# Kernel tuning notes

Measured on AMD Instinct MI355X. Metric: run time of the kernel, lower is better.

## Reference

```python
import jax, jax.numpy as jnp
import numpy as np

HEAD_CHOICES = [8, 10, 12]
MAX_HEADS = 12
HEAD_DIM = 64
MAX_REL_POS = 14
SCALE = HEAD_DIM ** -0.5


def _rel_indices(N):
    # AutoFormer RelativePosition2D_super index computation (static, numpy).
    L = N - 1                      # remove cls token
    s = int(L ** 0.5)              # patches per row
    r = np.arange(L)
    dv = r[None, :] // s - r[:, None] // s
    dh = r[None, :] % s - r[:, None] % s
    iv = np.clip(dv, -MAX_REL_POS, MAX_REL_POS) + MAX_REL_POS + 1
    ih = np.clip(dh, -MAX_REL_POS, MAX_REL_POS) + MAX_REL_POS + 1
    iv = np.pad(iv, ((1, 0), (1, 0)))  # cls token row/col -> index 0
    ih = np.pad(ih, ((1, 0), (1, 0)))
    return jnp.asarray(iv), jnp.asarray(ih)


def setup_inputs() -> dict:
    key = jax.random.key(0)
    ks = jax.random.split(key, 6)
    B, N = 16, 577
    T = 2 * MAX_REL_POS + 2  # 30
    x = jax.random.normal(ks[0], (B, N, 3 * MAX_HEADS * HEAD_DIM), dtype=jnp.float32)
    weights = jax.nn.softmax(jax.random.normal(ks[1], (len(HEAD_CHOICES),), dtype=jnp.float32))
    rel_k_table_v = jax.random.normal(ks[2], (T, HEAD_DIM), dtype=jnp.float32) * 0.02
    rel_k_table_h = jax.random.normal(ks[3], (T, HEAD_DIM), dtype=jnp.float32) * 0.02
    rel_v_table_v = jax.random.normal(ks[4], (T, HEAD_DIM), dtype=jnp.float32) * 0.02
    rel_v_table_h = jax.random.normal(ks[5], (T, HEAD_DIM), dtype=jnp.float32) * 0.02
    return dict(x=x, weights=weights,
                rel_k_table_v=rel_k_table_v, rel_k_table_h=rel_k_table_h,
                rel_v_table_v=rel_v_table_v, rel_v_table_h=rel_v_table_h)


def reference(x, weights, rel_k_table_v, rel_k_table_h, rel_v_table_v, rel_v_table_h):
    B, N, _ = x.shape
    # [3, B, H, N, D]
    qkv = x.reshape(B, N, 3, MAX_HEADS, HEAD_DIM).transpose(2, 0, 3, 1, 4)
    # Mixture over head-count choices: slicing first c heads, scaling by w[i],
    # padding to max_heads, and summing == per-head weight sum_i w[i]*[h < c_i].
    head_mask = jnp.asarray(np.array([[1.0 if h < c else 0.0 for h in range(MAX_HEADS)]
                                      for c in HEAD_CHOICES]), dtype=x.dtype)  # [C, H]
    w_head = weights @ head_mask  # [H]
    w4 = w_head[None, :, None, None]
    q = qkv[0] * w4
    k = qkv[1] * w4
    v = qkv[2] * w4
    # content attention + relative-position K bias
    attn = jnp.einsum('bhnd,bhmd->bhnm', q, k) * SCALE
    iv, ih = _rel_indices(N)
    rel_k = rel_k_table_v[iv] + rel_k_table_h[ih]  # [N, N, D]
    attn = attn + jnp.einsum('bhnd,nmd->bhnm', q, rel_k) * SCALE
    attn = jax.nn.softmax(attn, axis=-1)  # attn_drop has p=0 (eval)
    out = jnp.einsum('bhnm,bhmd->bhnd', attn, v)
    rel_v = rel_v_table_v[iv] + rel_v_table_h[ih]  # [N, N, D]
    out = out + jnp.einsum('bhnm,nmd->bhnd', attn, rel_v)
    return out.transpose(0, 2, 1, 3).reshape(B, N, MAX_HEADS * HEAD_DIM)
```

## Files before the change

kernel.cpp:

```cpp
#include <hip/hip_runtime.h>

typedef short bf16x8_t __attribute__((ext_vector_type(8)));
typedef float f32x4_t __attribute__((ext_vector_type(4)));

#define NTOK 577
#define QPAD 640
#define MPAD 608
#define NSTEP 19
#define VTILES 80
#define VTILE_ELEMS 6144

__device__ __forceinline__ unsigned short f2bf(float f) {
  unsigned u = __builtin_bit_cast(unsigned, f);
  u += 0x7FFFu + ((u >> 16) & 1u);
  return (unsigned short)(u >> 16);
}
__device__ __forceinline__ float headw(const float* wts, int h) {
  float w0 = wts[0], w1 = wts[1], w2 = wts[2];
  return (h < 8) ? (w0 + w1 + w2) : ((h < 10) ? (w1 + w2) : w2);
}
__device__ __forceinline__ unsigned rangemask(int lo, int hi) {
  lo = lo < 0 ? 0 : lo; hi = hi > 32 ? 32 : hi;
  if (hi <= lo) return 0u;
  unsigned mh = (hi >= 32) ? 0xFFFFFFFFu : ((1u << hi) - 1u);
  unsigned ml = (1u << lo) - 1u;
  return mh & ~ml;
}

extern "C" __global__ __launch_bounds__(256) void prep_x3(
    const float* __restrict__ x, const float* __restrict__ wts,
    unsigned short* __restrict__ qbf, unsigned short* __restrict__ kbf,
    unsigned short* __restrict__ vbf) {
  __shared__ unsigned short vT[8][768];
  const int tid = threadIdx.x;
  const int mc = blockIdx.x;
  const int n0 = mc * 8;
  const int b = blockIdx.y;
  const float w0 = wts[0], w1 = wts[1], w2 = wts[2];
  const float wA = w0 + w1 + w2, wB = w1 + w2, wC = w2;
  const float* xb = x + (size_t)b * NTOK * 2304;
#pragma unroll 2
  for (int p = 0; p < 18; ++p) {
    int i = p * 256 + tid;
    int nl = i / 576;
    int c4 = i - nl * 576;
    int n = n0 + nl;
    float4 v = {0.f, 0.f, 0.f, 0.f};
    if (n < NTOK) v = *(const float4*)(xb + (size_t)n * 2304 + c4 * 4);
    int sec = c4 / 192;
    int cc = c4 - sec * 192;
    int h = cc >> 4, d4 = cc & 15;
    if (sec == 2) {
      ushort4 o;
      o.x = f2bf(v.x); o.y = f2bf(v.y); o.z = f2bf(v.z); o.w = f2bf(v.w);
      *(ushort4*)&vT[nl][cc * 4] = o;
    } else {
      float s = 1.f;
      if (sec == 0) {
        float w = (h < 8) ? wA : ((h < 10) ? wB : wC);
        s = w * w * 0.125f;
      }
      ushort4 o;
      o.x = f2bf(v.x * s); o.y = f2bf(v.y * s); o.z = f2bf(v.z * s); o.w = f2bf(v.w * s);
      unsigned short* dst = (sec == 0) ? qbf : kbf;
      *(ushort4*)(dst + ((size_t)(b * 12 + h)) * QPAD * 64 + (size_t)n * 64 + d4 * 4) = o;
    }
  }
  __syncthreads();
  unsigned short* tile = vbf + (size_t)(b * VTILES + mc) * VTILE_ELEMS;
#pragma unroll
  for (int t = 0; t < 3; ++t) {
    int hd = t * 256 + tid;
    bf16x8_t val;
#pragma unroll
    for (int jj = 0; jj < 8; ++jj) val[jj] = (short)vT[jj][hd];
    *(bf16x8_t*)(tile + (size_t)hd * 8) = val;
  }
}

extern "C" __global__ __launch_bounds__(256) void prep_tab(
    const float* __restrict__ wts,
    const float* __restrict__ tkv, const float* __restrict__ tkh,
    const float* __restrict__ tvv, const float* __restrict__ tvh,
    unsigned short* __restrict__ tkb, unsigned short* __restrict__ tvb,
    unsigned short* __restrict__ gfb) {
  int tid = threadIdx.x, bx = blockIdx.x;
  if (bx < 48) {
    int cid = bx * 256 + tid;
    int d4 = cid & 15, t = (cid >> 4) & 31, tb = (cid >> 9) & 1, h = cid >> 10;
    float s = 1.f / headw(wts, h);
    const float* src = tb ? tkh : tkv;
    float4 v = {0,0,0,0};
    if (t < 30) v = *(const float4*)(src + t * 64 + d4 * 4);
    ushort4 o;
    o.x = f2bf(v.x * s); o.y = f2bf(v.y * s); o.z = f2bf(v.z * s); o.w = f2bf(v.w * s);
    *(ushort4*)(tkb + (((size_t)(h * 2 + tb)) * 32 + t) * 64 + d4 * 4) = o;
  } else if (bx == 48) {
    for (int i = 0; i < 16; ++i) {
      int id = tid * 16 + i;
      int t = id & 31, d = (id >> 5) & 63, tb = id >> 11;
      const float* src = tb ? tvh : tvv;
      tvb[id] = (t < 30) ? f2bf(src[t * 64 + d]) : (unsigned short)0;
    }
  } else {
    int id = (bx - 49) * 256 + tid;
    int lane = id & 63, gt = (id >> 6) & 1;
    int sg = id >> 7;
    int step = sg % 19, tb = sg / 19;
    int l15 = lane & 15, quad = lane >> 4;
    int g = gt * 16 + l15;
    int m0 = step * 32;
    unsigned mask = 0u;
    if (g < 25) {
      if (g == 24) {
        mask = rangemask(NTOK - m0, MPAD - m0);
        if (step == 0) mask |= 1u;
      } else if (tb == 0) {
        mask = rangemask(24 * g + 1 - m0, 24 * g + 25 - m0);
      } else {
        int j0 = (g + 1 - m0) % 24; if (j0 < 0) j0 += 24;
        for (int j = j0; j < 32; j += 24) {
          int m = m0 + j;
          if (m >= 1 && m < NTOK) mask |= (1u << j);
        }
      }
    }
    unsigned short o[8];
#pragma unroll
    for (int j = 0; j < 8; ++j) {
      int m_loc = quad * 8 + j;
      o[j] = ((mask >> m_loc) & 1u) ? (unsigned short)0x3F80 : (unsigned short)0;
    }
    *(ushort4*)(gfb + (size_t)id * 8) = *(ushort4*)&o[0];
    *(ushort4*)(gfb + (size_t)id * 8 + 4) = *(ushort4*)&o[4];
  }
}

struct __align__(16) SMem {
  float qg_t[2][25][68];
  float l_s[64];
  union {
    struct { float qv_t[2][64][30]; } pro;
    struct { unsigned short P_s[2][64][44]; } loop;
    struct { float sv_f[2][64][30]; } epi;
  } u;
};

extern "C" __global__ __launch_bounds__(256, 4) void hma_kernel(
    const unsigned short* __restrict__ qbf, const unsigned short* __restrict__ kbf,
    const unsigned short* __restrict__ vbf, const unsigned short* __restrict__ tkb,
    const unsigned short* __restrict__ tvb, const unsigned short* __restrict__ gfb,
    const float* __restrict__ wts, float* __restrict__ out) {
  __shared__ SMem sm;
  const int tid = threadIdx.x;
  const int wave = tid >> 6, lane = tid & 63, quad = lane >> 4, l15 = lane & 15;
  const int rg = wave & 1;
  const int cg = wave >> 1;
  const int tb_w = cg;
  const int nwg = gridDim.x * gridDim.y * gridDim.z;
  const int L = blockIdx.x + gridDim.x * (blockIdx.y + gridDim.y * blockIdx.z);
  const int wid = (L & 7) * (nwg >> 3) + (L >> 3);
  const int n0 = (wid % 10) * 64;
  const int rest = wid / 10;
  const int h = rest % 12, b = rest / 12;
  const float w = headw(wts, h);

  const unsigned short* qb = qbf + ((size_t)(b * 12 + h)) * QPAD * 64;
  const unsigned short* kb = kbf + ((size_t)(b * 12 + h)) * QPAD * 64;
  const unsigned short* gfp = gfb + ((size_t)tb_w * 19) * 1024 + lane * 8;

  bf16x8_t qa[2][2];
  for (int sub = 0; sub < 2; ++sub)
    for (int kk = 0; kk < 2; ++kk)
      qa[sub][kk] = *(const bf16x8_t*)(qb + (size_t)(n0 + rg * 32 + sub * 16 + l15) * 64 + kk * 32 + quad * 8);

  {
    const unsigned short* tkp = tkb + ((size_t)(h * 2 + tb_w)) * 32 * 64;
    for (int tt = 0; tt < 2; ++tt) {
      for (int sub = 0; sub < 2; ++sub) {
        f32x4_t acc = {0.f, 0.f, 0.f, 0.f};
        for (int kk = 0; kk < 2; ++kk) {
          bf16x8_t bb = *(const bf16x8_t*)(tkp + (size_t)(tt * 16 + l15) * 64 + kk * 32 + quad * 8);
          acc = __builtin_amdgcn_mfma_f32_16x16x32_bf16(qa[sub][kk], bb, acc, 0, 0, 0);
        }
        int t = tt * 16 + l15;
        if (t < 30)
          for (int r = 0; r < 4; ++r)
            sm.u.pro.qv_t[tb_w][rg * 32 + sub * 16 + quad * 4 + r][t] = acc[r];
      }
    }
  }
  __syncthreads();
  for (int p = tid; p < 2 * 25 * 64; p += 256) {
    int tb = p / 1600, r2 = p % 1600, g = r2 / 64, n = r2 % 64;
    int n_g = n0 + n;
    int t;
    if (n_g == 0 || n_g >= NTOK || g == 24) t = 0;
    else {
      int base = tb ? ((n_g - 1) % 24) : ((n_g - 1) / 24);
      int dq = g - base; dq = dq < -14 ? -14 : (dq > 14 ? 14 : dq);
      t = dq + 15;
    }
    sm.qg_t[tb][g][n] = sm.u.pro.qv_t[tb][n][t];
  }
  __syncthreads();

  const int m_loc = cg * 16 + l15;
  int rmv, cmv;
  if (m_loc == 0) { rmv = 0; cmv = -1; }
  else { rmv = (m_loc - 1) / 24; cmv = (m_loc - 1) - rmv * 24; }
  const bool cls_lane = (m_loc == 0);

  f32x4_t oacc[2][2] = {{{0,0,0,0},{0,0,0,0}},{{0,0,0,0},{0,0,0,0}}};
  f32x4_t rsacc[2][2] = {{{0,0,0,0},{0,0,0,0}},{{0,0,0,0},{0,0,0,0}}};

  const unsigned short* kfr = kb + (size_t)(cg * 16 + l15) * 64 + quad * 8;
  const unsigned short* vfr = vbf + (size_t)b * VTILES * VTILE_ELEMS + h * 512
                              + (size_t)(cg * 32 + l15) * 8;
  bf16x8_t kf0 = *(const bf16x8_t*)(kfr);
  bf16x8_t kf1 = *(const bf16x8_t*)(kfr + 32);

  for (int step = 0; step < NSTEP; ++step) {
    const int m0 = step * 32;
    const int buf = step & 1;
    bf16x8_t gv0 = *(const bf16x8_t*)(gfp + (size_t)step * 1024);
    bf16x8_t gv1 = *(const bf16x8_t*)(gfp + (size_t)step * 1024 + 512);
    f32x4_t s[2] = {{0,0,0,0},{0,0,0,0}};
    for (int sub = 0; sub < 2; ++sub) {
      s[sub] = __builtin_amdgcn_mfma_f32_16x16x32_bf16(qa[sub][0], kf0, s[sub], 0, 0, 0);
      s[sub] = __builtin_amdgcn_mfma_f32_16x16x32_bf16(qa[sub][1], kf1, s[sub], 0, 0, 0);
    }
    const unsigned short* vt = vfr + (size_t)(m0 / 8 + quad) * VTILE_ELEMS;
    bf16x8_t vf0 = *(const bf16x8_t*)(vt);
    bf16x8_t vf1 = *(const bf16x8_t*)(vt + 128);
    kf0 = *(const bf16x8_t*)(kfr + (size_t)(m0 + 32) * 64);
    kf1 = *(const bf16x8_t*)(kfr + (size_t)(m0 + 32) * 64 + 32);
    const int m_g = m0 + m_loc;
    int ur = rmv, uc = cmv;
    if (cls_lane && step == 0) { ur = 24; uc = 24; }
    const bool mpad = (m_g >= NTOK);
    for (int sub = 0; sub < 2; ++sub) {
      int nbase = rg * 32 + sub * 16 + quad * 4;
      f32x4_t g0 = *(const f32x4_t*)&sm.qg_t[0][ur][nbase];
      f32x4_t g1 = *(const f32x4_t*)&sm.qg_t[1][uc][nbase];
      for (int r = 0; r < 4; ++r) {
        float logit = s[sub][r] + g0[r] + g1[r];
        float p = __expf(logit);
        if (mpad) p = 0.f;
        unsigned u = __builtin_bit_cast(unsigned, p);
        sm.u.loop.P_s[buf][nbase + r][m_loc] = (unsigned short)((u + 0x8000u) >> 16);
      }
    }
    { int c = cmv + 8; int carry = (c >= 24); cmv = carry ? c - 24 : c; rmv += 1 + carry; }
    __syncthreads();
    bf16x8_t pa[2];
    for (int sub = 0; sub < 2; ++sub)
      pa[sub] = *(const bf16x8_t*)&sm.u.loop.P_s[buf][rg * 32 + sub * 16 + l15][quad * 8];
    for (int sub = 0; sub < 2; ++sub) {
      oacc[sub][0] = __builtin_amdgcn_mfma_f32_16x16x32_bf16(pa[sub], vf0, oacc[sub][0], 0, 0, 0);
      oacc[sub][1] = __builtin_amdgcn_mfma_f32_16x16x32_bf16(pa[sub], vf1, oacc[sub][1], 0, 0, 0);
    }
    for (int sub = 0; sub < 2; ++sub) {
      rsacc[sub][0] = __builtin_amdgcn_mfma_f32_16x16x32_bf16(pa[sub], gv0, rsacc[sub][0], 0, 0, 0);
      rsacc[sub][1] = __builtin_amdgcn_mfma_f32_16x16x32_bf16(pa[sub], gv1, rsacc[sub][1], 0, 0, 0);
    }
  }

  __syncthreads();
  for (int e = tid; e < 2 * 64 * 30; e += 256) (&sm.u.epi.sv_f[0][0][0])[e] = 0.f;
  __syncthreads();
  for (int sub = 0; sub < 2; ++sub)
    for (int gt = 0; gt < 2; ++gt) {
      int g = gt * 16 + l15;
      if (g < 25) {
        for (int r = 0; r < 4; ++r) {
          int n_loc = rg * 32 + sub * 16 + quad * 4 + r;
          int n_g = n0 + n_loc;
          int t;
          if (n_g == 0 || n_g >= NTOK || g == 24) t = 0;
          else {
            int base = tb_w ? ((n_g - 1) % 24) : ((n_g - 1) / 24);
            int dq = g - base; dq = dq < -14 ? -14 : (dq > 14 ? 14 : dq);
            t = dq + 15;
          }
          atomicAdd(&sm.u.epi.sv_f[tb_w][n_loc][t], rsacc[sub][gt][r]);
        }
      }
    }
  __syncthreads();
  if (tid < 64) {
    float l = 0.f;
    for (int t = 0; t < 30; ++t) l += sm.u.epi.sv_f[0][tid][t];
    sm.l_s[tid] = l;
  }
  for (int sub = 0; sub < 2; ++sub)
    for (int ds = 0; ds < 2; ++ds)
      for (int r = 0; r < 4; ++r) oacc[sub][ds][r] *= w;
  for (int tb = 0; tb < 2; ++tb) {
    bf16x8_t av[2];
    for (int sub = 0; sub < 2; ++sub) {
      int n_loc = rg * 32 + sub * 16 + l15;
      for (int j = 0; j < 8; ++j) {
        int t = quad * 8 + j;
        float f = (t < 30) ? sm.u.epi.sv_f[tb][n_loc][t] : 0.f;
        unsigned u = __builtin_bit_cast(unsigned, f);
        av[sub][j] = (short)((u + 0x8000u) >> 16);
      }
    }
    for (int ds = 0; ds < 2; ++ds) {
      bf16x8_t bb = *(const bf16x8_t*)(tvb + ((size_t)(tb * 64 + cg * 32 + ds * 16 + l15)) * 32 + quad * 8);
      for (int sub = 0; sub < 2; ++sub)
        oacc[sub][ds] = __builtin_amdgcn_mfma_f32_16x16x32_bf16(av[sub], bb, oacc[sub][ds], 0, 0, 0);
    }
  }
  __syncthreads();
  float* ob = out + (size_t)b * NTOK * 768 + h * 64;
  for (int sub = 0; sub < 2; ++sub)
    for (int r = 0; r < 4; ++r) {
      int n_loc = rg * 32 + sub * 16 + quad * 4 + r;
      int n_g = n0 + n_loc;
      if (n_g < NTOK) {
        float inv = 1.f / sm.l_s[n_loc];
        for (int ds = 0; ds < 2; ++ds) {
          int d = cg * 32 + ds * 16 + l15;
          ob[(size_t)n_g * 768 + d] = oacc[sub][ds][r] * inv;
        }
      }
    }
}

extern "C" void kernel_launch(void* const* d_in, const int* in_sizes, int n_in,
                              void* d_out, int out_size, void* d_ws, size_t ws_size,
                              hipStream_t stream) {
  const float* x   = (const float*)d_in[0];
  const float* wts = (const float*)d_in[1];
  const float* tkv = (const float*)d_in[2];
  const float* tkh = (const float*)d_in[3];
  const float* tvv = (const float*)d_in[4];
  const float* tvh = (const float*)d_in[5];
  float* out = (float*)d_out;
  const int B = in_sizes[0] / (NTOK * 2304);

  unsigned short* ws = (unsigned short*)d_ws;
  size_t qkSz = (size_t)B * 12 * QPAD * 64;
  unsigned short* qbf = ws;
  unsigned short* kbf = ws + qkSz;
  unsigned short* vbf = ws + 2 * qkSz;
  unsigned short* tkb = vbf + qkSz;
  unsigned short* tvb = tkb + (size_t)12 * 2 * 32 * 64;
  unsigned short* gfb = tvb + (size_t)2 * 64 * 32;

  prep_x3<<<dim3(VTILES, B), 256, 0, stream>>>(x, wts, qbf, kbf, vbf);
  prep_tab<<<dim3(68, 1, 1), 256, 0, stream>>>(wts, tkv, tkh, tvv, tvh, tkb, tvb, gfb);
  hma_kernel<<<dim3(10, 12, B), 256, 0, stream>>>(qbf, kbf, vbf, tkb, tvb, gfb, wts, out);
}
```

Measured before the change: 251.4 us.

## Halve shared-memory union via sequential tb passes, raise occupancy, use exp2

The prologue and epilogue scratch arrays used to hold both relative-position directions at once. They now hold one direction, processed in two sequential passes, which shrinks the shared-memory union. Launch bounds go from 4 to 6 blocks per CU to take advantage of the smaller footprint. Separately, log2(e) is folded into the Q scale so the softmax can use exp2 directly. The cost is extra barriers and passes in the prologue and epilogue, plus tighter register limits that could cause spills.

Result: slower. 341.3 us (+35.7%).

```diff
diff --git a/kernel.cpp b/kernel.cpp
--- a/kernel.cpp
+++ b/kernel.cpp
@@ -9,6 +9,7 @@
 #define NSTEP 19
 #define VTILES 80
 #define VTILE_ELEMS 6144
+#define LOG2E 1.44269504088896340736f
 
 __device__ __forceinline__ unsigned short f2bf(float f) {
   unsigned u = __builtin_bit_cast(unsigned, f);
@@ -58,7 +59,7 @@
       float s = 1.f;
       if (sec == 0) {
         float w = (h < 8) ? wA : ((h < 10) ? wB : wC);
-        s = w * w * 0.125f;
+        s = w * w * 0.125f * LOG2E;
       }
       ushort4 o;
       o.x = f2bf(v.x * s); o.y = f2bf(v.y * s); o.z = f2bf(v.z * s); o.w = f2bf(v.w * s);
@@ -140,13 +141,13 @@
   float qg_t[2][25][68];
   float l_s[64];
   union {
-    struct { float qv_t[2][64][30]; } pro;
+    struct { float qv_t[64][30]; } pro;
     struct { unsigned short P_s[2][64][44]; } loop;
-    struct { float sv_f[2][64][30]; } epi;
+    struct { float sv_f[64][30]; } epi;
   } u;
 };
 
-extern "C" __global__ __launch_bounds__(256, 4) void hma_kernel(
+extern "C" __global__ __launch_bounds__(256, 6) void hma_kernel(
     const unsigned short* __restrict__ qbf, const unsigned short* __restrict__ kbf,
     const unsigned short* __restrict__ vbf, const unsigned short* __restrict__ tkb,
     const unsigned short* __restrict__ tvb, const unsigned short* __restrict__ gfb,
@@ -174,36 +175,35 @@
     for (int kk = 0; kk < 2; ++kk)
       qa[sub][kk] = *(const bf16x8_t*)(qb + (size_t)(n0 + rg * 32 + sub * 16 + l15) * 64 + kk * 32 + quad * 8);
 
-  {
-    const unsigned short* tkp = tkb + ((size_t)(h * 2 + tb_w)) * 32 * 64;
-    for (int tt = 0; tt < 2; ++tt) {
-      for (int sub = 0; sub < 2; ++sub) {
-        f32x4_t acc = {0.f, 0.f, 0.f, 0.f};
-        for (int kk = 0; kk < 2; ++kk) {
-          bf16x8_t bb = *(const bf16x8_t*)(tkp + (size_t)(tt * 16 + l15) * 64 + kk * 32 + quad * 8);
-          acc = __builtin_amdgcn_mfma_f32_16x16x32_bf16(qa[sub][kk], bb, acc, 0, 0, 0);
-        }
-        int t = tt * 16 + l15;
-        if (t < 30)
-          for (int r = 0; r < 4; ++r)
-            sm.u.pro.qv_t[tb_w][rg * 32 + sub * 16 + quad * 4 + r][t] = acc[r];
-      }
-    }
-  }
-  __syncthreads();
-  for (int p = tid; p < 2 * 25 * 64; p += 256) {
-    int tb = p / 1600, r2 = p % 1600, g = r2 / 64, n = r2 % 64;
-    int n_g = n0 + n;
-    int t;
-    if (n_g == 0 || n_g >= NTOK || g == 24) t = 0;
-    else {
-      int base = tb ? ((n_g - 1) % 24) : ((n_g - 1) / 24);
-      int dq = g - base; dq = dq < -14 ? -14 : (dq > 14 ? 14 : dq);
-      t = dq + 15;
-    }
-    sm.qg_t[tb][g][n] = sm.u.pro.qv_t[tb][n][t];
-  }
-  __syncthreads();
+  for (int tb = 0; tb < 2; ++tb) {
+    const unsigned short* tkp = tkb + ((size_t)(h * 2 + tb)) * 32 * 64;
+    const int tt = cg;
+    for (int sub = 0; sub < 2; ++sub) {
+      f32x4_t acc = {0.f, 0.f, 0.f, 0.f};
+      for (int kk = 0; kk < 2; ++kk) {
+        bf16x8_t bb = *(const bf16x8_t*)(tkp + (size_t)(tt * 16 + l15) * 64 + kk * 32 + quad * 8);
+        acc = __builtin_amdgcn_mfma_f32_16x16x32_bf16(qa[sub][kk], bb, acc, 0, 0, 0);
+      }
+      int t = tt * 16 + l15;
+      if (t < 30)
+        for (int r = 0; r < 4; ++r)
+          sm.u.pro.qv_t[rg * 32 + sub * 16 + quad * 4 + r][t] = acc[r];
+    }
+    __syncthreads();
+    for (int p = tid; p < 25 * 64; p += 256) {
+      int g = p / 64, n = p % 64;
+      int n_g = n0 + n;
+      int t;
+      if (n_g == 0 || n_g >= NTOK || g == 24) t = 0;
+      else {
+        int base = tb ? ((n_g - 1) % 24) : ((n_g - 1) / 24);
+        int dq = g - base; dq = dq < -14 ? -14 : (dq > 14 ? 14 : dq);
+        t = dq + 15;
+      }
+      sm.qg_t[tb][g][n] = sm.u.pro.qv_t[n][t];
+    }
+    __syncthreads();
+  }
 
   const int m_loc = cg * 16 + l15;
   int rmv, cmv;
@@ -245,7 +245,7 @@
       f32x4_t g1 = *(const f32x4_t*)&sm.qg_t[1][uc][nbase];
       for (int r = 0; r < 4; ++r) {
         float logit = s[sub][r] + g0[r] + g1[r];
-        float p = __expf(logit);
+        float p = __builtin_exp2f(logit);
         if (mpad) p = 0.f;
         unsigned u = __builtin_bit_cast(unsigned, p);
         sm.u.loop.P_s[buf][nbase + r][m_loc] = (unsigned short)((u + 0x8000u) >> 16);
@@ -267,42 +267,46 @@
   }
 
   __syncthreads();
-  for (int e = tid; e < 2 * 64 * 30; e += 256) (&sm.u.epi.sv_f[0][0][0])[e] = 0.f;
-  __syncthreads();
-  for (int sub = 0; sub < 2; ++sub)
-    for (int gt = 0; gt < 2; ++gt) {
-      int g = gt * 16 + l15;
-      if (g < 25) {
-        for (int r = 0; r < 4; ++r) {
-          int n_loc = rg * 32 + sub * 16 + quad * 4 + r;
-          int n_g = n0 + n_loc;
-          int t;
-          if (n_g == 0 || n_g >= NTOK || g == 24) t = 0;
-          else {
-            int base = tb_w ? ((n_g - 1) % 24) : ((n_g - 1) / 24);
-            int dq = g - base; dq = dq < -14 ? -14 : (dq > 14 ? 14 : dq);
-            t = dq + 15;
+  for (int tb = 0; tb < 2; ++tb) {
+    for (int e = tid; e < 64 * 30; e += 256) (&sm.u.epi.sv_f[0][0])[e] = 0.f;
+    __syncthreads();
+    if (cg == tb) {
+      for (int sub = 0; sub < 2; ++sub)
+        for (int gt = 0; gt < 2; ++gt) {
+          int g = gt * 16 + l15;
+          if (g < 25) {
+            for (int r = 0; r < 4; ++r) {
+              int n_loc = rg * 32 + sub * 16 + quad * 4 + r;
+              int n_g = n0 + n_loc;
+              int t;
+              if (n_g == 0 || n_g >= NTOK || g == 24) t = 0;
+              else {
+                int base = tb ? ((n_g - 1) % 24) : ((n_g - 1) / 24);
+                int dq = g - base; dq = dq < -14 ? -14 : (dq > 14 ? 14 : dq);
+                t = dq + 15;
+              }
+              atomicAdd(&sm.u.epi.sv_f[n_loc][t], rsacc[sub][gt][r]);
+            }
           }
-          atomicAdd(&sm.u.epi.sv_f[tb_w][n_loc][t], rsacc[sub][gt][r]);
         }
-      }
-    }
-  __syncthreads();
-  if (tid < 64) {
-    float l = 0.f;
-    for (int t = 0; t < 30; ++t) l += sm.u.epi.sv_f[0][tid][t];
-    sm.l_s[tid] = l;
-  }
-  for (int sub = 0; sub < 2; ++sub)
-    for (int ds = 0; ds < 2; ++ds)
-      for (int r = 0; r < 4; ++r) oacc[sub][ds][r] *= w;
-  for (int tb = 0; tb < 2; ++tb) {
+    }
+    __syncthreads();
+    if (tb == 0) {
+      if (tid < 64) {
+        float l = 0.f;
+        for (int t = 0; t < 30; ++t) l += sm.u.epi.sv_f[tid][t];
+        sm.l_s[tid] = l;
+      }
+      for (int sub = 0; sub < 2; ++sub)
+        for (int ds = 0; ds < 2; ++ds)
+          for (int r = 0; r < 4; ++r) oacc[sub][ds][r] *= w;
+    }
     bf16x8_t av[2];
     for (int sub = 0; sub < 2; ++sub) {
       int n_loc = rg * 32 + sub * 16 + l15;
       for (int j = 0; j < 8; ++j) {
         int t = quad * 8 + j;
-        float f = (t < 30) ? sm.u.epi.sv_f[tb][n_loc][t] : 0.f;
+        float f = (t < 30) ? sm.u.epi.sv_f[n_loc][t] : 0.f;
         unsigned u = __builtin_bit_cast(unsigned, f);
         av[sub][j] = (short)((u + 0x8000u) >> 16);
       }
@@ -312,8 +316,8 @@
       for (int sub = 0; sub < 2; ++sub)
         oacc[sub][ds] = __builtin_amdgcn_mfma_f32_16x16x32_bf16(av[sub], bb, oacc[sub][ds], 0, 0, 0);
     }
-  }
-  __syncthreads();
+    __syncthreads();
+  }
   float* ob = out + (size_t)b * NTOK * 768 + h * 64;
   for (int sub = 0; sub < 2; ++sub)
     for (int r = 0; r < 4; ++r) {
```
